# Kernel tuning notes

Measured on AMD Instinct MI355X. Metric: run time of the kernel, lower is better.

The kernel has to match this reference:

```python
import jax, jax.numpy as jnp
import numpy as np
from jax import lax

START_TAG = 29
STOP_TAG = 30
PAD_TAG = 31
NEG_INF = -10000.0


def setup_inputs() -> dict:
    key = jax.random.key(0)
    k_feat, k_trans, k_len = jax.random.split(key, 3)
    S, B, T = 1024, 1024, 32
    feats = jax.random.normal(k_feat, (S, B, T), dtype=jnp.float32)
    # left-aligned padding mask with random lengths in [S//2, S]
    lengths = jax.random.randint(k_len, (B,), S // 2, S + 1)
    mask = (jnp.arange(S)[:, None] < lengths[None, :]).astype(jnp.float32)  # [S,B]
    transitions = jax.random.normal(k_trans, (T, T), dtype=jnp.float32)
    # replicate the constraint initialization from __init__
    transitions = transitions.at[START_TAG, :].set(NEG_INF)
    transitions = transitions.at[:, STOP_TAG].set(NEG_INF)
    transitions = transitions.at[:, PAD_TAG].set(NEG_INF)
    transitions = transitions.at[PAD_TAG, :].set(NEG_INF)
    transitions = transitions.at[PAD_TAG, STOP_TAG].set(0.0)
    transitions = transitions.at[PAD_TAG, PAD_TAG].set(0.0)
    # zero emissions at padded steps, as _get_lstm_features does (feats * mask)
    feats = feats * mask[:, :, None]
    return {"feats": feats, "mask": mask, "transitions": transitions}


def reference(feats, mask, transitions):
    """CRF forward algorithm (log partition) + Viterbi max-score scan.

    feats: [S, B, T] emission scores, mask: [S, B] float, transitions: [T, T]
    (transitions[i, j] = score of transitioning from tag j to tag i).
    Returns (logZ [B], best_score [B], pointers [S, B, T] int32).
    """
    S, B, T = feats.shape

    alpha0 = jnp.full((B, T), NEG_INF, dtype=feats.dtype).at[:, START_TAG].set(0.0)

    def fwd_step(alpha, xs):
        feat, m = xs  # feat [B,T], m [B]
        # alpha_t[b, i, j] = alpha[b, j] + transitions[i, j] + feat[b, i]
        alpha_t = alpha[:, None, :] + transitions[None, :, :] + feat[:, :, None]
        new = jax.nn.logsumexp(alpha_t, axis=-1)  # [B,T]
        m = m[:, None]
        return new * m + alpha * (1.0 - m), None

    alpha, _ = lax.scan(fwd_step, alpha0, (feats, mask))
    logZ = jax.nn.logsumexp(alpha + transitions[STOP_TAG][None, :], axis=-1)  # [B]

    def vit_step(scores, xs):
        feat, m = xs
        scores_t = scores[:, None, :] + transitions[None, :, :]  # [B,T,T]
        best = jnp.max(scores_t, axis=-1)                        # [B,T]
        ptr = jnp.argmax(scores_t, axis=-1).astype(jnp.int32)    # [B,T]
        scores_t = best + feat
        m = m[:, None]
        return scores_t * m + scores * (1.0 - m), ptr

    scores0 = jnp.full((B, T), NEG_INF, dtype=feats.dtype).at[:, START_TAG].set(0.0)
    scores, pointers = lax.scan(vit_step, scores0, (feats, mask))
    scores = scores + transitions[STOP_TAG][None, :]
    best_score = jnp.max(scores, axis=-1)  # [B]
    return logZ, best_score, pointers
```

## Files before the change

kernel.cpp:

```cpp
#include <hip/hip_runtime.h>


#define SS 1024
#define BB 1024
#define TT 32
#define POFF (2 * BB)
#define STEP (BB * TT)

#define DPP_QX1   0xB1
#define DPP_QX2   0x4E
#define DPP_QX3   0x1B
#define DPP_RMIR  0x140
#define DPP_RHMIR 0x141
#define DPP_ROR8  0x128

template <int CTRL>
static __device__ __forceinline__ float dppx(float x) {
  return __int_as_float(
      __builtin_amdgcn_update_dpp(0, __float_as_int(x), CTRL, 0xF, 0xF, false));
}

static __device__ __forceinline__ float swap32(float x, bool hiHalf) {
#if __has_builtin(__builtin_amdgcn_permlane32_swap)
  auto r = __builtin_amdgcn_permlane32_swap(__float_as_uint(x),
                                            __float_as_uint(x), false, false);
  return __uint_as_float(hiHalf ? r[0] : r[1]);
#else
  float a = x, b = x;
  asm("s_nop 1\n\ts_nop 1\n\tv_permlane32_swap_b32 %0, %1"
      : "+v"(a), "+v"(b));
  return hiHalf ? a : b;
#endif
}

static __device__ __forceinline__ float swap16(float x, bool hi16) {
#if __has_builtin(__builtin_amdgcn_permlane16_swap)
  auto r = __builtin_amdgcn_permlane16_swap(__float_as_uint(x),
                                            __float_as_uint(x), false, false);
  return __uint_as_float(hi16 ? r[0] : r[1]);
#else
  float a = x, b = x;
  asm("s_nop 1\n\ts_nop 1\n\tv_permlane16_swap_b32 %0, %1"
      : "+v"(a), "+v"(b));
  return hi16 ? a : b;
#endif
}

__global__ __launch_bounds__(64, 2) void crf8_kernel(
    const float* __restrict__ feats,
    const float* __restrict__ mask,
    const float* __restrict__ trans,
    float* __restrict__ out) {

  const int l   = threadIdx.x;
  const int t0  = l & 15;
  const int row = l >> 4;
  const int i   = ((row & 1) << 4) | t0;
  const int srcbase = (row == 1 || row == 2) ? 16 : 0;
  const bool hi16   = (row & 1) != 0;
  const bool hiHalf = (row & 2) != 0;
  const int b = blockIdx.x;

  const float* fbase = feats + (size_t)b * TT + i;
  const float t_stop = trans[30 * TT + i];

  float fA[4], fB[4];
#pragma unroll
  for (int u = 0; u < 4; ++u) {
    fA[u] = fbase[(size_t)u * STEP];
    fB[u] = fbase[(size_t)(u + 4) * STEP];
  }

  int len;
  {
    float pr1 = mask[(size_t)(l << 4) * BB + b];
    unsigned long long m1 = __ballot(pr1 != 0.0f);
    unsigned long long nz = ~m1;
    int z1 = nz ? (__ffsll(nz) - 1) : 64;
    int W = (z1 << 4) - 16;
    float pr2 = mask[(size_t)(W + t0) * BB + b];
    unsigned long long m2 = __ballot(pr2 != 0.0f);
    len = W + __popcll(m2 & 0xFFFFull);
  }
  const int lim8 = len & ~7;
  const int rem  = len - lim8;

  if (blockIdx.y == 0) {
    float eT[16];
#pragma unroll
    for (int m = 0; m < 16; ++m)
      eT[m] = __expf(trans[i * TT + (srcbase | (t0 ^ m))]);

    float p   = (i == 29) ? 1.0f : 0.0f;
    int   CE  = 0;
    float q0f = 1.0f;

    auto fstep = [&](float fv) {
      float ef = __expf(fv);
      int Eb = (int)((__float_as_uint(q0f) >> 23) & 0xFFu);
      float scl = __uint_as_float((unsigned)(254 - Eb) << 23);
      float efs = ef * scl;
      float z = swap16(p, hi16);
      float x = hiHalf ? z : p;
      float r7  = dppx<DPP_RHMIR>(x);
      float r8  = dppx<DPP_ROR8>(x);
      float r15 = dppx<DPP_RMIR>(x);
      float a0 = eT[0] * x;
      float a1 = eT[1] * dppx<DPP_QX1>(x);
      float a2 = eT[2] * dppx<DPP_QX2>(x);
      float a3 = eT[3] * dppx<DPP_QX3>(x);
      a0 = fmaf(dppx<DPP_QX3>(r7),  eT[4],  a0);
      a1 = fmaf(dppx<DPP_QX2>(r7),  eT[5],  a1);
      a2 = fmaf(dppx<DPP_QX1>(r7),  eT[6],  a2);
      a3 = fmaf(r7,                 eT[7],  a3);
      a0 = fmaf(r8,                 eT[8],  a0);
      a1 = fmaf(dppx<DPP_QX1>(r8),  eT[9],  a1);
      a2 = fmaf(dppx<DPP_QX2>(r8),  eT[10], a2);
      a3 = fmaf(dppx<DPP_QX3>(r8),  eT[11], a3);
      a0 = fmaf(dppx<DPP_QX3>(r15), eT[12], a0);
      a1 = fmaf(dppx<DPP_QX2>(r15), eT[13], a1);
      a2 = fmaf(dppx<DPP_QX1>(r15), eT[14], a2);
      a3 = fmaf(r15,                eT[15], a3);
      float Dp = (a0 + a1) + (a2 + a3);
      float Df = Dp + swap32(Dp, hiHalf);
      p = Df * efs;
      CE += Eb - 127;
      q0f = __uint_as_float(
          (unsigned)__builtin_amdgcn_readfirstlane((int)__float_as_uint(p)));
    };

#pragma unroll 1
    for (int s = 0; s < lim8; s += 8) {
      fstep(fA[0]); fstep(fA[1]); fstep(fA[2]); fstep(fA[3]);
#pragma unroll
      for (int u = 0; u < 4; ++u)
        fA[u] = fbase[(size_t)((s + 8 + u) & (SS - 1)) * STEP];
      fstep(fB[0]); fstep(fB[1]); fstep(fB[2]); fstep(fB[3]);
#pragma unroll
      for (int u = 0; u < 4; ++u)
        fB[u] = fbase[(size_t)((s + 12 + u) & (SS - 1)) * STEP];
    }
    if (rem > 0) fstep(fA[0]);
    if (rem > 1) fstep(fA[1]);
    if (rem > 2) fstep(fA[2]);
    if (rem > 3) fstep(fA[3]);
    if (rem > 4) fstep(fB[0]);
    if (rem > 5) fstep(fB[1]);
    if (rem > 6) fstep(fB[2]);
    {
      float alpha = (float)CE * 0.693147180559945f + __logf(p);
      float v = alpha + t_stop;
      float M2 = v;
      M2 = fmaxf(M2, __shfl_xor(M2, 1, 64));
      M2 = fmaxf(M2, __shfl_xor(M2, 2, 64));
      M2 = fmaxf(M2, __shfl_xor(M2, 4, 64));
      M2 = fmaxf(M2, __shfl_xor(M2, 8, 64));
      M2 = fmaxf(M2, __shfl_xor(M2, 16, 64));
      float e = __expf(v - M2);
      e += __shfl_xor(e, 1, 64);
      e += __shfl_xor(e, 2, 64);
      e += __shfl_xor(e, 4, 64);
      e += __shfl_xor(e, 8, 64);
      e += __shfl_xor(e, 16, 64);
      if (l == 0) out[b] = M2 + __logf(e);
    }
    return;
  }

  {
    float tT[16];
    unsigned tg[16];
#pragma unroll
    for (int m = 0; m < 16; ++m) {
      int j = srcbase | (t0 ^ m);
      tT[m] = trans[i * TT + j];
      tg[m] = (unsigned)j;
    }

    float sc = (i == 29) ? 0.0f : -10000.0f;
    float* outp = out + POFF + (size_t)b * TT + i;

    auto vstep = [&](float& best, int& ptr) {
      float z = swap16(sc, hi16);
      float x = hiHalf ? z : sc;
      float r7  = dppx<DPP_RHMIR>(x);
      float r8  = dppx<DPP_ROR8>(x);
      float r15 = dppx<DPP_RMIR>(x);
      float vv[16];
      vv[0]  = x + tT[0];
      vv[1]  = dppx<DPP_QX1>(x) + tT[1];
      vv[2]  = dppx<DPP_QX2>(x) + tT[2];
      vv[3]  = dppx<DPP_QX3>(x) + tT[3];
      vv[4]  = dppx<DPP_QX3>(r7) + tT[4];
      vv[5]  = dppx<DPP_QX2>(r7) + tT[5];
      vv[6]  = dppx<DPP_QX1>(r7) + tT[6];
      vv[7]  = r7 + tT[7];
      vv[8]  = r8 + tT[8];
      vv[9]  = dppx<DPP_QX1>(r8) + tT[9];
      vv[10] = dppx<DPP_QX2>(r8) + tT[10];
      vv[11] = dppx<DPP_QX3>(r8) + tT[11];
      vv[12] = dppx<DPP_QX3>(r15) + tT[12];
      vv[13] = dppx<DPP_QX2>(r15) + tT[13];
      vv[14] = dppx<DPP_QX1>(r15) + tT[14];
      vv[15] = r15 + tT[15];
      float g0 = fmaxf(fmaxf(vv[0], vv[1]), vv[2]);
      float g1 = fmaxf(fmaxf(vv[3], vv[4]), vv[5]);
      float g2 = fmaxf(fmaxf(vv[6], vv[7]), vv[8]);
      float g3 = fmaxf(fmaxf(vv[9], vv[10]), vv[11]);
      float g4 = fmaxf(fmaxf(vv[12], vv[13]), vv[14]);
      float h0 = fmaxf(fmaxf(g0, g1), g2);
      float h1 = fmaxf(fmaxf(g3, g4), vv[15]);
      float mxp = fmaxf(h0, h1);
      float mx  = fmaxf(mxp, swap32(mxp, hiHalf));
      unsigned k[16];
#pragma unroll
      for (int m = 0; m < 16; ++m) k[m] = (vv[m] == mx) ? tg[m] : 63u;
      unsigned n0 = min(min(k[0],  k[1]),  k[2]);
      unsigned n1 = min(min(k[3],  k[4]),  k[5]);
      unsigned n2 = min(min(k[6],  k[7]),  k[8]);
      unsigned n3 = min(min(k[9],  k[10]), k[11]);
      unsigned n4 = min(min(k[12], k[13]), k[14]);
      unsigned p0 = min(min(n0, n1), n2);
      unsigned p1 = min(min(n3, n4), k[15]);
      int idx = (int)min(p0, p1);
      int oidx = __float_as_int(swap32(__int_as_float(idx), hiHalf));
      idx = (oidx < idx) ? oidx : idx;
      best = mx;
      ptr  = idx;
    };

#pragma unroll 1
    for (int s = 0; s < lim8; s += 8) {
#pragma unroll
      for (int u2 = 0; u2 < 4; ++u2) {
        float best; int ptr;
        vstep(best, ptr);
        if (l < 32) outp[(size_t)(s + u2) * STEP] = (float)ptr;
        sc = best + fA[u2];
      }
#pragma unroll
      for (int u2 = 0; u2 < 4; ++u2)
        fA[u2] = fbase[(size_t)((s + 8 + u2) & (SS - 1)) * STEP];
#pragma unroll
      for (int u2 = 0; u2 < 4; ++u2) {
        float best; int ptr;
        vstep(best, ptr);
        if (l < 32) outp[(size_t)(s + 4 + u2) * STEP] = (float)ptr;
        sc = best + fB[u2];
      }
#pragma unroll
      for (int u2 = 0; u2 < 4; ++u2)
        fB[u2] = fbase[(size_t)((s + 12 + u2) & (SS - 1)) * STEP];
    }
    {
      float tf[7] = {fA[0], fA[1], fA[2], fA[3], fB[0], fB[1], fB[2]};
#pragma unroll 1
      for (int k2 = 0; k2 < rem; ++k2) {
        float best; int ptr;
        vstep(best, ptr);
        if (l < 32) outp[(size_t)(lim8 + k2) * STEP] = (float)ptr;
        sc = best + tf[k2];
      }
    }
    {
      float tb; int tp;
      vstep(tb, tp);
      float tj = (float)tp;
#pragma unroll 1
      for (int s2 = len; s2 < SS; ++s2)
        if (l < 32) outp[(size_t)s2 * STEP] = tj;

      float w = sc + t_stop;
      w = fmaxf(w, __shfl_xor(w, 1, 64));
      w = fmaxf(w, __shfl_xor(w, 2, 64));
      w = fmaxf(w, __shfl_xor(w, 4, 64));
      w = fmaxf(w, __shfl_xor(w, 8, 64));
      w = fmaxf(w, __shfl_xor(w, 16, 64));
      if (l == 0) out[BB + b] = w;
    }
  }
}

extern "C" void kernel_launch(void* const* d_in, const int* in_sizes, int n_in,
                              void* d_out, int out_size, void* d_ws, size_t ws_size,
                              hipStream_t stream) {
  const float* feats = (const float*)d_in[0];
  const float* msk   = (const float*)d_in[1];
  const float* trans = (const float*)d_in[2];
  float* out = (float*)d_out;
  (void)in_sizes; (void)n_in; (void)out_size; (void)d_ws; (void)ws_size;
  crf8_kernel<<<dim3(BB, 2), dim3(64), 0, stream>>>(feats, msk, trans, out);
}
```

Baseline: 547.7 us.

## Fuse forward and Viterbi recurrences into one wave per batch with bitmask argmax

Merges the two per-batch blocks (forward logsumexp and Viterbi) into a single 64-lane wave that advances both recurrences in the same step loop. The goal is to share the feature loads and length detection and to interleave two independent dependency chains, hiding DPP and permlane latency. The argmax is now a 32-bit bitmask merged across halves and resolved with ffs, replacing the min-reduction tree. The cost is half as many waves in flight (1024 instead of 2048) and more registers per wave, with launch bounds relaxed to 1.

Result: slower. 604.6 us (+10.4%).

```diff
diff --git a/kernel.cpp b/kernel.cpp
--- a/kernel.cpp
+++ b/kernel.cpp
@@ -20,17 +20,19 @@
       __builtin_amdgcn_update_dpp(0, __float_as_int(x), CTRL, 0xF, 0xF, false));
 }
 
-static __device__ __forceinline__ float swap32(float x, bool hiHalf) {
+static __device__ __forceinline__ unsigned uswap32(unsigned x, bool hiHalf) {
 #if __has_builtin(__builtin_amdgcn_permlane32_swap)
-  auto r = __builtin_amdgcn_permlane32_swap(__float_as_uint(x),
-                                            __float_as_uint(x), false, false);
-  return __uint_as_float(hiHalf ? r[0] : r[1]);
+  auto r = __builtin_amdgcn_permlane32_swap(x, x, false, false);
+  return hiHalf ? r[0] : r[1];
 #else
-  float a = x, b = x;
+  unsigned a = x, b = x;
   asm("s_nop 1\n\ts_nop 1\n\tv_permlane32_swap_b32 %0, %1"
       : "+v"(a), "+v"(b));
   return hiHalf ? a : b;
 #endif
+}
+static __device__ __forceinline__ float swap32(float x, bool hiHalf) {
+  return __uint_as_float(uswap32(__float_as_uint(x), hiHalf));
 }
 
 static __device__ __forceinline__ float swap16(float x, bool hi16) {
@@ -46,7 +48,7 @@
 #endif
 }
 
-__global__ __launch_bounds__(64, 2) void crf8_kernel(
+__global__ __launch_bounds__(64, 1) void crf9_kernel(
     const float* __restrict__ feats,
     const float* __restrict__ mask,
     const float* __restrict__ trans,
@@ -85,199 +87,184 @@
   const int lim8 = len & ~7;
   const int rem  = len - lim8;
 
-  if (blockIdx.y == 0) {
-    float eT[16];
-#pragma unroll
-    for (int m = 0; m < 16; ++m)
-      eT[m] = __expf(trans[i * TT + (srcbase | (t0 ^ m))]);
-
-    float p   = (i == 29) ? 1.0f : 0.0f;
-    int   CE  = 0;
-    float q0f = 1.0f;
-
-    auto fstep = [&](float fv) {
-      float ef = __expf(fv);
-      int Eb = (int)((__float_as_uint(q0f) >> 23) & 0xFFu);
-      float scl = __uint_as_float((unsigned)(254 - Eb) << 23);
-      float efs = ef * scl;
-      float z = swap16(p, hi16);
-      float x = hiHalf ? z : p;
-      float r7  = dppx<DPP_RHMIR>(x);
-      float r8  = dppx<DPP_ROR8>(x);
-      float r15 = dppx<DPP_RMIR>(x);
-      float a0 = eT[0] * x;
-      float a1 = eT[1] * dppx<DPP_QX1>(x);
-      float a2 = eT[2] * dppx<DPP_QX2>(x);
-      float a3 = eT[3] * dppx<DPP_QX3>(x);
-      a0 = fmaf(dppx<DPP_QX3>(r7),  eT[4],  a0);
-      a1 = fmaf(dppx<DPP_QX2>(r7),  eT[5],  a1);
-      a2 = fmaf(dppx<DPP_QX1>(r7),  eT[6],  a2);
-      a3 = fmaf(r7,                 eT[7],  a3);
-      a0 = fmaf(r8,                 eT[8],  a0);
-      a1 = fmaf(dppx<DPP_QX1>(r8),  eT[9],  a1);
-      a2 = fmaf(dppx<DPP_QX2>(r8),  eT[10], a2);
-      a3 = fmaf(dppx<DPP_QX3>(r8),  eT[11], a3);
-      a0 = fmaf(dppx<DPP_QX3>(r15), eT[12], a0);
-      a1 = fmaf(dppx<DPP_QX2>(r15), eT[13], a1);
-      a2 = fmaf(dppx<DPP_QX1>(r15), eT[14], a2);
-      a3 = fmaf(r15,                eT[15], a3);
-      float Dp = (a0 + a1) + (a2 + a3);
-      float Df = Dp + swap32(Dp, hiHalf);
-      p = Df * efs;
-      CE += Eb - 127;
-      q0f = __uint_as_float(
-          (unsigned)__builtin_amdgcn_readfirstlane((int)__float_as_uint(p)));
-    };
+  float eT[16], tT[16];
+  unsigned tgb[16];
+#pragma unroll
+  for (int m = 0; m < 16; ++m) {
+    int j = srcbase | (t0 ^ m);
+    float tv = trans[i * TT + j];
+    tT[m]  = tv;
+    eT[m]  = __expf(tv);
+    tgb[m] = 1u << j;
+  }
+
+  float p   = (i == 29) ? 1.0f : 0.0f;
+  int   CE  = 0;
+  float q0f = 1.0f;
+  float sc  = (i == 29) ? 0.0f : -10000.0f;
+  float* outp = out + POFF + (size_t)b * TT + i;
+
+  auto step = [&](float fv, int s) {
+    float zv = swap16(sc, hi16);
+    float xv = hiHalf ? zv : sc;
+    float v7  = dppx<DPP_RHMIR>(xv);
+    float v8  = dppx<DPP_ROR8>(xv);
+    float v15 = dppx<DPP_RMIR>(xv);
+    float vv[16];
+    vv[0]  = xv + tT[0];
+    vv[1]  = dppx<DPP_QX1>(xv) + tT[1];
+    vv[2]  = dppx<DPP_QX2>(xv) + tT[2];
+    vv[3]  = dppx<DPP_QX3>(xv) + tT[3];
+    vv[4]  = dppx<DPP_QX3>(v7) + tT[4];
+    vv[5]  = dppx<DPP_QX2>(v7) + tT[5];
+    vv[6]  = dppx<DPP_QX1>(v7) + tT[6];
+    vv[7]  = v7 + tT[7];
+    vv[8]  = v8 + tT[8];
+    vv[9]  = dppx<DPP_QX1>(v8) + tT[9];
+    vv[10] = dppx<DPP_QX2>(v8) + tT[10];
+    vv[11] = dppx<DPP_QX3>(v8) + tT[11];
+    vv[12] = dppx<DPP_QX3>(v15) + tT[12];
+    vv[13] = dppx<DPP_QX2>(v15) + tT[13];
+    vv[14] = dppx<DPP_QX1>(v15) + tT[14];
+    vv[15] = v15 + tT[15];
+    float g0 = fmaxf(fmaxf(vv[0], vv[1]), vv[2]);
+    float g1 = fmaxf(fmaxf(vv[3], vv[4]), vv[5]);
+    float g2 = fmaxf(fmaxf(vv[6], vv[7]), vv[8]);
+    float g3 = fmaxf(fmaxf(vv[9], vv[10]), vv[11]);
+    float g4 = fmaxf(fmaxf(vv[12], vv[13]), vv[14]);
+    float h0 = fmaxf(fmaxf(g0, g1), g2);
+    float h1 = fmaxf(fmaxf(g3, g4), vv[15]);
+    float mxp = fmaxf(h0, h1);
+    float mx  = fmaxf(mxp, swap32(mxp, hiHalf));
+    unsigned msk = 0u;
+#pragma unroll
+    for (int m = 0; m < 16; ++m) msk |= (vv[m] == mx) ? tgb[m] : 0u;
+    msk |= uswap32(msk, hiHalf);
+    int ptr = __ffs(msk) - 1;
+    if (l < 32) outp[(size_t)s * STEP] = (float)ptr;
+
+    float ef = __expf(fv);
+    int Eb = (int)((__float_as_uint(q0f) >> 23) & 0xFFu);
+    float scl = __uint_as_float((unsigned)(254 - Eb) << 23);
+    float efs = ef * scl;
+    float zp = swap16(p, hi16);
+    float xp = hiHalf ? zp : p;
+    float r7  = dppx<DPP_RHMIR>(xp);
+    float r8  = dppx<DPP_ROR8>(xp);
+    float r15 = dppx<DPP_RMIR>(xp);
+    float a0 = eT[0] * xp;
+    float a1 = eT[1] * dppx<DPP_QX1>(xp);
+    float a2 = eT[2] * dppx<DPP_QX2>(xp);
+    float a3 = eT[3] * dppx<DPP_QX3>(xp);
+    a0 = fmaf(dppx<DPP_QX3>(r7),  eT[4],  a0);
+    a1 = fmaf(dppx<DPP_QX2>(r7),  eT[5],  a1);
+    a2 = fmaf(dppx<DPP_QX1>(r7),  eT[6],  a2);
+    a3 = fmaf(r7,                 eT[7],  a3);
+    a0 = fmaf(r8,                 eT[8],  a0);
+    a1 = fmaf(dppx<DPP_QX1>(r8),  eT[9],  a1);
+    a2 = fmaf(dppx<DPP_QX2>(r8),  eT[10], a2);
+    a3 = fmaf(dppx<DPP_QX3>(r8),  eT[11], a3);
+    a0 = fmaf(dppx<DPP_QX3>(r15), eT[12], a0);
+    a1 = fmaf(dppx<DPP_QX2>(r15), eT[13], a1);
+    a2 = fmaf(dppx<DPP_QX1>(r15), eT[14], a2);
+    a3 = fmaf(r15,                eT[15], a3);
+    float Dp = (a0 + a1) + (a2 + a3);
+    float Df = Dp + swap32(Dp, hiHalf);
+    p = Df * efs;
+    CE += Eb - 127;
+    q0f = __uint_as_float(
+        (unsigned)__builtin_amdgcn_readfirstlane((int)__float_as_uint(p)));
+
+    sc = mx + fv;
+  };
 
 #pragma unroll 1
-    for (int s = 0; s < lim8; s += 8) {
-      fstep(fA[0]); fstep(fA[1]); fstep(fA[2]); fstep(fA[3]);
-#pragma unroll
-      for (int u = 0; u < 4; ++u)
-        fA[u] = fbase[(size_t)((s + 8 + u) & (SS - 1)) * STEP];
-      fstep(fB[0]); fstep(fB[1]); fstep(fB[2]); fstep(fB[3]);
-#pragma unroll
-      for (int u = 0; u < 4; ++u)
-        fB[u] = fbase[(size_t)((s + 12 + u) & (SS - 1)) * STEP];
-    }
-    if (rem > 0) fstep(fA[0]);
-    if (rem > 1) fstep(fA[1]);
-    if (rem > 2) fstep(fA[2]);
-    if (rem > 3) fstep(fA[3]);
-    if (rem > 4) fstep(fB[0]);
-    if (rem > 5) fstep(fB[1]);
-    if (rem > 6) fstep(fB[2]);
-    {
-      float alpha = (float)CE * 0.693147180559945f + __logf(p);
-      float v = alpha + t_stop;
-      float M2 = v;
-      M2 = fmaxf(M2, __shfl_xor(M2, 1, 64));
-      M2 = fmaxf(M2, __shfl_xor(M2, 2, 64));
-      M2 = fmaxf(M2, __shfl_xor(M2, 4, 64));
-      M2 = fmaxf(M2, __shfl_xor(M2, 8, 64));
-      M2 = fmaxf(M2, __shfl_xor(M2, 16, 64));
-      float e = __expf(v - M2);
-      e += __shfl_xor(e, 1, 64);
-      e += __shfl_xor(e, 2, 64);
-      e += __shfl_xor(e, 4, 64);
-      e += __shfl_xor(e, 8, 64);
-      e += __shfl_xor(e, 16, 64);
-      if (l == 0) out[b] = M2 + __logf(e);
-    }
-    return;
-  }
+  for (int s = 0; s < lim8; s += 8) {
+    step(fA[0], s);     step(fA[1], s + 1);
+    step(fA[2], s + 2); step(fA[3], s + 3);
+#pragma unroll
+    for (int u = 0; u < 4; ++u)
+      fA[u] = fbase[(size_t)((s + 8 + u) & (SS - 1)) * STEP];
+    step(fB[0], s + 4); step(fB[1], s + 5);
+    step(fB[2], s + 6); step(fB[3], s + 7);
+#pragma unroll
+    for (int u = 0; u < 4; ++u)
+      fB[u] = fbase[(size_t)((s + 12 + u) & (SS - 1)) * STEP];
+  }
+  if (rem > 0) step(fA[0], lim8 + 0);
+  if (rem > 1) step(fA[1], lim8 + 1);
+  if (rem > 2) step(fA[2], lim8 + 2);
+  if (rem > 3) step(fA[3], lim8 + 3);
+  if (rem > 4) step(fB[0], lim8 + 4);
+  if (rem > 5) step(fB[1], lim8 + 5);
+  if (rem > 6) step(fB[2], lim8 + 6);
 
   {
-    float tT[16];
-    unsigned tg[16];
-#pragma unroll
-    for (int m = 0; m < 16; ++m) {
-      int j = srcbase | (t0 ^ m);
-      tT[m] = trans[i * TT + j];
-      tg[m] = (unsigned)j;
-    }
-
-    float sc = (i == 29) ? 0.0f : -10000.0f;
-    float* outp = out + POFF + (size_t)b * TT + i;
-
-    auto vstep = [&](float& best, int& ptr) {
-      float z = swap16(sc, hi16);
-      float x = hiHalf ? z : sc;
-      float r7  = dppx<DPP_RHMIR>(x);
-      float r8  = dppx<DPP_ROR8>(x);
-      float r15 = dppx<DPP_RMIR>(x);
-      float vv[16];
-      vv[0]  = x + tT[0];
-      vv[1]  = dppx<DPP_QX1>(x) + tT[1];
-      vv[2]  = dppx<DPP_QX2>(x) + tT[2];
-      vv[3]  = dppx<DPP_QX3>(x) + tT[3];
-      vv[4]  = dppx<DPP_QX3>(r7) + tT[4];
-      vv[5]  = dppx<DPP_QX2>(r7) + tT[5];
-      vv[6]  = dppx<DPP_QX1>(r7) + tT[6];
-      vv[7]  = r7 + tT[7];
-      vv[8]  = r8 + tT[8];
-      vv[9]  = dppx<DPP_QX1>(r8) + tT[9];
-      vv[10] = dppx<DPP_QX2>(r8) + tT[10];
-      vv[11] = dppx<DPP_QX3>(r8) + tT[11];
-      vv[12] = dppx<DPP_QX3>(r15) + tT[12];
-      vv[13] = dppx<DPP_QX2>(r15) + tT[13];
-      vv[14] = dppx<DPP_QX1>(r15) + tT[14];
-      vv[15] = r15 + tT[15];
-      float g0 = fmaxf(fmaxf(vv[0], vv[1]), vv[2]);
-      float g1 = fmaxf(fmaxf(vv[3], vv[4]), vv[5]);
-      float g2 = fmaxf(fmaxf(vv[6], vv[7]), vv[8]);
-      float g3 = fmaxf(fmaxf(vv[9], vv[10]), vv[11]);
-      float g4 = fmaxf(fmaxf(vv[12], vv[13]), vv[14]);
-      float h0 = fmaxf(fmaxf(g0, g1), g2);
-      float h1 = fmaxf(fmaxf(g3, g4), vv[15]);
-      float mxp = fmaxf(h0, h1);
-      float mx  = fmaxf(mxp, swap32(mxp, hiHalf));
-      unsigned k[16];
-#pragma unroll
-      for (int m = 0; m < 16; ++m) k[m] = (vv[m] == mx) ? tg[m] : 63u;
-      unsigned n0 = min(min(k[0],  k[1]),  k[2]);
-      unsigned n1 = min(min(k[3],  k[4]),  k[5]);
-      unsigned n2 = min(min(k[6],  k[7]),  k[8]);
-      unsigned n3 = min(min(k[9],  k[10]), k[11]);
-      unsigned n4 = min(min(k[12], k[13]), k[14]);
-      unsigned p0 = min(min(n0, n1), n2);
-      unsigned p1 = min(min(n3, n4), k[15]);
-      int idx = (int)min(p0, p1);
-      int oidx = __float_as_int(swap32(__int_as_float(idx), hiHalf));
-      idx = (oidx < idx) ? oidx : idx;
-      best = mx;
-      ptr  = idx;
-    };
-
+    float zv = swap16(sc, hi16);
+    float xv = hiHalf ? zv : sc;
+    float v7  = dppx<DPP_RHMIR>(xv);
+    float v8  = dppx<DPP_ROR8>(xv);
+    float v15 = dppx<DPP_RMIR>(xv);
+    float vv[16];
+    vv[0]  = xv + tT[0];
+    vv[1]  = dppx<DPP_QX1>(xv) + tT[1];
+    vv[2]  = dppx<DPP_QX2>(xv) + tT[2];
+    vv[3]  = dppx<DPP_QX3>(xv) + tT[3];
+    vv[4]  = dppx<DPP_QX3>(v7) + tT[4];
+    vv[5]  = dppx<DPP_QX2>(v7) + tT[5];
+    vv[6]  = dppx<DPP_QX1>(v7) + tT[6];
+    vv[7]  = v7 + tT[7];
+    vv[8]  = v8 + tT[8];
+    vv[9]  = dppx<DPP_QX1>(v8) + tT[9];
+    vv[10] = dppx<DPP_QX2>(v8) + tT[10];
+    vv[11] = dppx<DPP_QX3>(v8) + tT[11];
+    vv[12] = dppx<DPP_QX3>(v15) + tT[12];
+    vv[13] = dppx<DPP_QX2>(v15) + tT[13];
+    vv[14] = dppx<DPP_QX1>(v15) + tT[14];
+    vv[15] = v15 + tT[15];
+    float g0 = fmaxf(fmaxf(vv[0], vv[1]), vv[2]);
+    float g1 = fmaxf(fmaxf(vv[3], vv[4]), vv[5]);
+    float g2 = fmaxf(fmaxf(vv[6], vv[7]), vv[8]);
+    float g3 = fmaxf(fmaxf(vv[9], vv[10]), vv[11]);
+    float g4 = fmaxf(fmaxf(vv[12], vv[13]), vv[14]);
+    float h0 = fmaxf(fmaxf(g0, g1), g2);
+    float h1 = fmaxf(fmaxf(g3, g4), vv[15]);
+    float mxp = fmaxf(h0, h1);
+    float mx  = fmaxf(mxp, swap32(mxp, hiHalf));
+    unsigned msk = 0u;
+#pragma unroll
+    for (int m = 0; m < 16; ++m) msk |= (vv[m] == mx) ? tgb[m] : 0u;
+    msk |= uswap32(msk, hiHalf);
+    float tj = (float)(__ffs(msk) - 1);
 #pragma unroll 1
-    for (int s = 0; s < lim8; s += 8) {
-#pragma unroll
-      for (int u2 = 0; u2 < 4; ++u2) {
-        float best; int ptr;
-        vstep(best, ptr);
-        if (l < 32) outp[(size_t)(s + u2) * STEP] = (float)ptr;
-        sc = best + fA[u2];
-      }
-#pragma unroll
-      for (int u2 = 0; u2 < 4; ++u2)
-        fA[u2] = fbase[(size_t)((s + 8 + u2) & (SS - 1)) * STEP];
-#pragma unroll
-      for (int u2 = 0; u2 < 4; ++u2) {
-        float best; int ptr;
-        vstep(best, ptr);
-        if (l < 32) outp[(size_t)(s + 4 + u2) * STEP] = (float)ptr;
-        sc = best + fB[u2];
-      }
-#pragma unroll
-      for (int u2 = 0; u2 < 4; ++u2)
-        fB[u2] = fbase[(size_t)((s + 12 + u2) & (SS - 1)) * STEP];
-    }
-    {
-      float tf[7] = {fA[0], fA[1], fA[2], fA[3], fB[0], fB[1], fB[2]};
-#pragma unroll 1
-      for (int k2 = 0; k2 < rem; ++k2) {
-        float best; int ptr;
-        vstep(best, ptr);
-        if (l < 32) outp[(size_t)(lim8 + k2) * STEP] = (float)ptr;
-        sc = best + tf[k2];
-      }
-    }
-    {
-      float tb; int tp;
-      vstep(tb, tp);
-      float tj = (float)tp;
-#pragma unroll 1
-      for (int s2 = len; s2 < SS; ++s2)
-        if (l < 32) outp[(size_t)s2 * STEP] = tj;
-
-      float w = sc + t_stop;
-      w = fmaxf(w, __shfl_xor(w, 1, 64));
-      w = fmaxf(w, __shfl_xor(w, 2, 64));
-      w = fmaxf(w, __shfl_xor(w, 4, 64));
-      w = fmaxf(w, __shfl_xor(w, 8, 64));
-      w = fmaxf(w, __shfl_xor(w, 16, 64));
-      if (l == 0) out[BB + b] = w;
-    }
+    for (int s2 = len; s2 < SS; ++s2)
+      if (l < 32) outp[(size_t)s2 * STEP] = tj;
+  }
+
+  {
+    float alpha = (float)CE * 0.693147180559945f + __logf(p);
+    float v = alpha + t_stop;
+    float M2 = v;
+    M2 = fmaxf(M2, __shfl_xor(M2, 1, 64));
+    M2 = fmaxf(M2, __shfl_xor(M2, 2, 64));
+    M2 = fmaxf(M2, __shfl_xor(M2, 4, 64));
+    M2 = fmaxf(M2, __shfl_xor(M2, 8, 64));
+    M2 = fmaxf(M2, __shfl_xor(M2, 16, 64));
+    float e = __expf(v - M2);
+    e += __shfl_xor(e, 1, 64);
+    e += __shfl_xor(e, 2, 64);
+    e += __shfl_xor(e, 4, 64);
+    e += __shfl_xor(e, 8, 64);
+    e += __shfl_xor(e, 16, 64);
+    if (l == 0) out[b] = M2 + __logf(e);
+
+    float w = sc + t_stop;
+    w = fmaxf(w, __shfl_xor(w, 1, 64));
+    w = fmaxf(w, __shfl_xor(w, 2, 64));
+    w = fmaxf(w, __shfl_xor(w, 4, 64));
+    w = fmaxf(w, __shfl_xor(w, 8, 64));
+    w = fmaxf(w, __shfl_xor(w, 16, 64));
+    if (l == 0) out[BB + b] = w;
   }
 }
 
@@ -289,5 +276,5 @@
   const float* trans = (const float*)d_in[2];
   float* out = (float*)d_out;
   (void)in_sizes; (void)n_in; (void)out_size; (void)d_ws; (void)ws_size;
-  crf8_kernel<<<dim3(BB, 2), dim3(64), 0, stream>>>(feats, msk, trans, out);
-}
+  crf9_kernel<<<dim3(BB), dim3(64), 0, stream>>>(feats, msk, trans, out);
+}
```
